# Performance work log

Hardware: AMD Instinct MI355X
Metric: run time of the kernel (lower is better)

## Reference

```python
import jax, jax.numpy as jnp
import numpy as np

KH = KW = 3          # kernel_size
PAD = 1              # padding (stride = 1)
K = KH * KW          # 9 kernel taps


def _bilinear_sample(x, ys, xs):
    """Bilinear sample with zero padding outside the image.
    x: [C,H,W]; ys, xs: [K,H,W] float sample coords. Returns [C,K,H,W]."""
    C, H, W = x.shape
    y0f = jnp.floor(ys)
    x0f = jnp.floor(xs)
    wy1 = ys - y0f
    wx1 = xs - x0f
    wy0 = 1.0 - wy1
    wx0 = 1.0 - wx1
    y0 = y0f.astype(jnp.int32)
    x0 = x0f.astype(jnp.int32)
    y1 = y0 + 1
    x1 = x0 + 1
    xf = x.reshape(C, H * W)

    def gather(yi, xi, wgt):
        valid = (yi >= 0) & (yi < H) & (xi >= 0) & (xi < W)
        idx = jnp.clip(yi, 0, H - 1) * W + jnp.clip(xi, 0, W - 1)  # [K,H,W]
        v = xf[:, idx.reshape(-1)].reshape(C, K, H, W)
        return v * (wgt * valid)[None]

    return (gather(y0, x0, wy0 * wx0) + gather(y0, x1, wy0 * wx1)
            + gather(y1, x0, wy1 * wx0) + gather(y1, x1, wy1 * wx1))


def _deform_conv2d(x, off, w):
    """DCNv1 for one (batch, group) slice.
    x: [C,H,W]; off: [2K,H,W] mmcv layout (dy,dx per tap); w: [Cout,Cin,KH,KW]."""
    C, H, W = x.shape
    off = off.reshape(K, 2, H, W)
    dy, dx = off[:, 0], off[:, 1]                       # [K,H,W]
    ky = (jnp.arange(K) // KW).astype(x.dtype)
    kx = (jnp.arange(K) % KW).astype(x.dtype)
    hh = jnp.arange(H, dtype=x.dtype)
    ww = jnp.arange(W, dtype=x.dtype)
    ys = dy + ky[:, None, None] - PAD + hh[None, :, None]   # stride=1
    xs = dx + kx[:, None, None] - PAD + ww[None, None, :]
    sampled = _bilinear_sample(x, ys, xs)               # [C,K,H,W]
    return jnp.einsum('ikhw,oik->ohw', sampled, w.reshape(w.shape[0], w.shape[1], K))


def reference(feat, offset, weight):
    """feat: [B,C,T,H,W]; offset: [B,2K,T,H,W]; weight: [T,Cout,Cin,KH,KW].
    groups=T, deform_groups=T -> each temporal slice is an independent DCN."""
    ft = jnp.transpose(feat, (0, 2, 1, 3, 4))    # [B,T,C,H,W]
    ot = jnp.transpose(offset, (0, 2, 1, 3, 4))  # [B,T,2K,H,W]
    per_t = jax.vmap(_deform_conv2d, in_axes=(0, 0, 0))       # over T (weight per-T)
    per_b = jax.vmap(per_t, in_axes=(0, 0, None))             # over B (weight shared)
    out = per_b(ft, ot, weight)                  # [B,T,C,H,W]
    return jnp.transpose(out, (0, 2, 1, 3, 4))   # [B,C,T,H,W]


def setup_inputs() -> dict:
    key = jax.random.key(0)
    k1, k2, k3 = jax.random.split(key, 3)
    B, C, T, H, W = 2, 32, 8, 192, 192
    feat = jax.random.normal(k1, (B, C, T, H, W), dtype=jnp.float32)
    offset = jax.random.normal(k2, (B, 2 * K, T, H, W), dtype=jnp.float32)
    weight = jax.random.normal(k3, (T, C, C, KH, KW), dtype=jnp.float32) * 0.05
    return {"feat": feat, "offset": offset, "weight": weight}
```

## Files before the change

### kernel.cpp

```cpp
#include <hip/hip_runtime.h>
#include <hip/hip_bf16.h>


#define CIN   32
#define COUT  32
#define TT    8
#define HH    192
#define WW    192
#define KK    9
#define HWSZ  (HH * WW)
#define PLANE (TT * HWSZ)

#define TILE_W 32
#define TILE_H 8
#define HALO   4
#define HROWS  (TILE_H + 2 * HALO + 1)
#define HCOLS  (TILE_W + 2 * HALO + 1)

typedef __attribute__((ext_vector_type(8))) short short8;
typedef __attribute__((ext_vector_type(4))) float f32x4;

union U4S8 { uint4 u; short8 s; };

__device__ __forceinline__ float bl_lo(uint u) { return __uint_as_float(u << 16); }
__device__ __forceinline__ float bl_hi(uint u) { return __uint_as_float(u & 0xffff0000u); }

__device__ __forceinline__ uint pk_bf16(float lo, float hi) {
    float2 p; p.x = lo; p.y = hi;
    __hip_bfloat162 b = __float22bfloat162_rn(p);
    union { __hip_bfloat162 b; uint u; } cv; cv.b = b;
    return cv.u;
}

__device__ __forceinline__ uint blerp_pack(uint a, uint b, uint c, uint d,
                                           float w00, float w01, float w10, float w11) {
    float lo = w00 * bl_lo(a) + w01 * bl_lo(b) + w10 * bl_lo(c) + w11 * bl_lo(d);
    float hi = w00 * bl_hi(a) + w01 * bl_hi(b) + w10 * bl_hi(c) + w11 * bl_hi(d);
    return pk_bf16(lo, hi);
}

__global__ __launch_bounds__(256) void transpose_bf16_kernel(
    const float* __restrict__ feat, uint* __restrict__ tf)
{
    __shared__ float tile[CIN][65];
    const int p0 = blockIdx.x * 64;
    const int t  = blockIdx.y;
    const int b  = blockIdx.z;

    const float* src = feat + (size_t)b * CIN * PLANE + (size_t)t * HWSZ + p0;
    #pragma unroll
    for (int it = 0; it < 8; ++it) {
        int i = it * 256 + threadIdx.x;
        int c = i >> 6, p = i & 63;
        tile[c][p] = src[(size_t)c * PLANE + p];
    }
    __syncthreads();

    uint* dst = tf + ((size_t)(b * TT + t) * HWSZ + p0) * (CIN / 2);
    #pragma unroll
    for (int it = 0; it < 4; ++it) {
        int i  = it * 256 + threadIdx.x;
        int p  = i >> 4, c2 = i & 15;
        dst[p * 16 + c2] = pk_bf16(tile[2 * c2][p], tile[2 * c2 + 1][p]);
    }
}

__global__ __launch_bounds__(256) void wprep_kernel(
    const float* __restrict__ wt, ushort* __restrict__ wfrag)
{
    int idx = blockIdx.x * 256 + threadIdx.x;
    if (idx >= TT * KK * 2 * 64 * 8) return;
    int t  = idx / (KK * 1024);
    int f  = idx % (KK * 1024);
    int k  = f >> 10;
    int r2 = f & 1023;
    int n    = r2 >> 9;
    int lane = (r2 >> 3) & 63;
    int j    = r2 & 7;
    int o = n * 16 + (lane & 15);
    int c = (lane >> 4) * 8 + j;
    float v = wt[(((size_t)t * COUT + o) * CIN + c) * KK + k];
    __hip_bfloat16 hb = __float2bfloat16(v);
    union { __hip_bfloat16 b; ushort u; } cv; cv.b = hb;
    wfrag[idx] = cv.u;
}

__global__ __launch_bounds__(256, 2) void dcn_mfma_kernel(
    const uint* __restrict__ tf,
    const float* __restrict__ offset,
    const ushort* __restrict__ wfrag,
    float* __restrict__ out)
{
    __shared__ uint4 halo[HROWS * HCOLS * 5];

    const int tid  = threadIdx.x;
    const int lane = tid & 63;
    const int wv   = tid >> 6;
    const int lane15 = lane & 15;
    const int quad   = lane >> 4;

    const int w0 = blockIdx.x * TILE_W;
    const int h0 = blockIdx.y * TILE_H;
    const int bt = blockIdx.z;
    const int t  = bt & (TT - 1);
    const int b  = bt >> 3;

    const int hlo = h0 - HALO, wlo = w0 - HALO;
    const int hhi = hlo + (HROWS - 1), whi = wlo + (HCOLS - 1);

    const uint4* tfs4 = (const uint4*)tf + (size_t)bt * HWSZ * 4;

    #pragma unroll
    for (int it = 0; it < 11; ++it) {
        int idx = it * 256 + tid;
        if (idx < HROWS * HCOLS * 4) {
            int r    = idx / (HCOLS * 4);
            int rem  = idx - r * (HCOLS * 4);
            int pv   = rem >> 2;
            int part = rem & 3;
            int gy = min(max(hlo + r, 0), HH - 1);
            int gx = min(max(wlo + pv, 0), WW - 1);
            halo[(r * HCOLS + pv) * 5 + part] = tfs4[(gy * WW + gx) * 4 + part];
        }
    }

    float offv[2 * KK];
    {
        const int orow = h0 + 2 * wv + (lane >> 5);
        const int ocol = w0 + (lane & 31);
        const float* offp = offset + (size_t)b * 2 * KK * PLANE
                          + (size_t)t * HWSZ + orow * WW + ocol;
        #pragma unroll
        for (int j = 0; j < 2 * KK; ++j) offv[j] = offp[(size_t)j * PLANE];
    }

    short8 bfr[KK][2];
    {
        const uint4* wfp = (const uint4*)(wfrag + (size_t)t * KK * 2 * 64 * 8);
        #pragma unroll
        for (int k = 0; k < KK; ++k)
            #pragma unroll
            for (int n = 0; n < 2; ++n) {
                U4S8 cv; cv.u = wfp[(k * 2 + n) * 64 + lane];
                bfr[k][n] = cv.s;
            }
    }

    __syncthreads();

    f32x4 acc[4][2];
    #pragma unroll
    for (int i = 0; i < 4; ++i)
        #pragma unroll
        for (int n = 0; n < 2; ++n) {
            acc[i][n][0] = 0.f; acc[i][n][1] = 0.f;
            acc[i][n][2] = 0.f; acc[i][n][3] = 0.f;
        }

    int own[4];
    #pragma unroll
    for (int i = 0; i < 4; ++i) own[i] = ((i >> 1) << 5) | ((i & 1) << 4) | lane15;

    #pragma unroll
    for (int k = 0; k < KK; ++k) {
        const int ky = k / 3 - 1;
        const int kx = k % 3 - 1;
        #pragma unroll
        for (int i = 0; i < 4; ++i) {
            const float dy = __shfl(offv[2 * k],     own[i], 64);
            const float dx = __shfl(offv[2 * k + 1], own[i], 64);
            const int hp = h0 + 2 * wv + (i >> 1);
            const int wp = w0 + ((i & 1) << 4) + lane15;

            const float ys = (float)(hp + ky) + dy;
            const float xs = (float)(wp + kx) + dx;
            const float y0f = floorf(ys), x0f = floorf(xs);
            const float wy1 = ys - y0f,  wx1 = xs - x0f;
            const float wy0 = 1.f - wy1, wx0 = 1.f - wx1;

            const int y0 = (int)y0f, x0i = (int)x0f;
            const int y1 = y0 + 1,   x1 = x0i + 1;

            const float vy0 = (y0 >= 0 && y0 < HH) ? 1.f : 0.f;
            const float vy1 = (y1 >= 0 && y1 < HH) ? 1.f : 0.f;
            const float vx0 = (x0i >= 0 && x0i < WW) ? 1.f : 0.f;
            const float vx1 = (x1 >= 0 && x1 < WW) ? 1.f : 0.f;

            const int cy0 = min(max(y0, 0), HH - 1);
            const int cy1 = min(max(y1, 0), HH - 1);
            const int cx0 = min(max(x0i, 0), WW - 1);
            const int cx1 = min(max(x1, 0), WW - 1);

            const float w00 = wy0 * wx0 * vy0 * vx0;
            const float w01 = wy0 * wx1 * vy0 * vx1;
            const float w10 = wy1 * wx0 * vy1 * vx0;
            const float w11 = wy1 * wx1 * vy1 * vx1;

            const bool inH = (cy0 >= hlo) & (cy1 <= hhi) & (cx0 >= wlo) & (cx1 <= whi);

            uint4 q00, q01, q10, q11;
            if (inH) {
                const int r0 = cy0 - hlo, r1 = cy1 - hlo;
                const int c0 = cx0 - wlo, c1 = cx1 - wlo;
                q00 = halo[(r0 * HCOLS + c0) * 5 + quad];
                q01 = halo[(r0 * HCOLS + c1) * 5 + quad];
                q10 = halo[(r1 * HCOLS + c0) * 5 + quad];
                q11 = halo[(r1 * HCOLS + c1) * 5 + quad];
            } else {
                q00 = tfs4[(cy0 * WW + cx0) * 4 + quad];
                q01 = tfs4[(cy0 * WW + cx1) * 4 + quad];
                q10 = tfs4[(cy1 * WW + cx0) * 4 + quad];
                q11 = tfs4[(cy1 * WW + cx1) * 4 + quad];
            }

            U4S8 af;
            af.u.x = blerp_pack(q00.x, q01.x, q10.x, q11.x, w00, w01, w10, w11);
            af.u.y = blerp_pack(q00.y, q01.y, q10.y, q11.y, w00, w01, w10, w11);
            af.u.z = blerp_pack(q00.z, q01.z, q10.z, q11.z, w00, w01, w10, w11);
            af.u.w = blerp_pack(q00.w, q01.w, q10.w, q11.w, w00, w01, w10, w11);

            acc[i][0] = __builtin_amdgcn_mfma_f32_16x16x32_bf16(af.s, bfr[k][0], acc[i][0], 0, 0, 0);
            acc[i][1] = __builtin_amdgcn_mfma_f32_16x16x32_bf16(af.s, bfr[k][1], acc[i][1], 0, 0, 0);
        }
    }

    float* ob = out + (size_t)b * COUT * PLANE + (size_t)t * HWSZ;
    #pragma unroll
    for (int i = 0; i < 4; ++i) {
        const int hp    = h0 + 2 * wv + (i >> 1);
        const int wbase = w0 + ((i & 1) << 4) + quad * 4;
        #pragma unroll
        for (int n = 0; n < 2; ++n) {
            const int o = n * 16 + lane15;
            float* op = ob + (size_t)o * PLANE + hp * WW + wbase;
            #pragma unroll
            for (int r = 0; r < 4; ++r) op[r] = acc[i][n][r];
        }
    }
}

__global__ __launch_bounds__(256) void dcn_fp32_kernel(
    const float* __restrict__ feat,
    const float* __restrict__ offset,
    const float* __restrict__ weight,
    float* __restrict__ out)
{
    __shared__ float sw[KK * CIN * COUT];
    const int tid = threadIdx.x;
    const int t   = blockIdx.y;
    const int b   = blockIdx.z;
    {
        const float* wg = weight + (size_t)t * (COUT * CIN * KK);
        #pragma unroll
        for (int j = 0; j < (KK * CIN * COUT) / 256; ++j) {
            int i  = tid + j * 256;
            int k  = i % KK;
            int oc = i / KK;
            sw[(k * CIN + (oc % CIN)) * COUT + (oc / CIN)] = wg[i];
        }
    }
    __syncthreads();

    const int pix = blockIdx.x * 256 + tid;
    const int h   = pix / WW;
    const int w   = pix % WW;

    float acc[COUT];
    #pragma unroll
    for (int o = 0; o < COUT; ++o) acc[o] = 0.0f;

    const float* offp = offset + ((size_t)(b * 2 * KK) * TT + t) * HWSZ + pix;
    float offv[2 * KK];
    #pragma unroll
    for (int j = 0; j < 2 * KK; ++j) offv[j] = offp[(size_t)j * PLANE];

    const float* fbase = feat + ((size_t)(b * CIN) * TT + t) * HWSZ;

    for (int k = 0; k < KK; ++k) {
        const float ys = (float)(h + k / 3 - 1) + offv[2 * k];
        const float xs = (float)(w + k % 3 - 1) + offv[2 * k + 1];
        const float y0f = floorf(ys), x0f = floorf(xs);
        const float wy1 = ys - y0f, wx1 = xs - x0f;
        const float wy0 = 1.0f - wy1, wx0 = 1.0f - wx1;
        const int y0 = (int)y0f, x0 = (int)x0f, y1 = y0 + 1, x1 = x0 + 1;
        const bool vy0 = (y0 >= 0) && (y0 < HH), vy1 = (y1 >= 0) && (y1 < HH);
        const bool vx0 = (x0 >= 0) && (x0 < WW), vx1 = (x1 >= 0) && (x1 < WW);
        const int cy0 = min(max(y0, 0), HH - 1), cy1 = min(max(y1, 0), HH - 1);
        const int cx0 = min(max(x0, 0), WW - 1), cx1 = min(max(x1, 0), WW - 1);
        const float w00 = wy0 * wx0 * ((vy0 && vx0) ? 1.0f : 0.0f);
        const float w01 = wy0 * wx1 * ((vy0 && vx1) ? 1.0f : 0.0f);
        const float w10 = wy1 * wx0 * ((vy1 && vx0) ? 1.0f : 0.0f);
        const float w11 = wy1 * wx1 * ((vy1 && vx1) ? 1.0f : 0.0f);
        const int i00 = cy0 * WW + cx0, i01 = cy0 * WW + cx1;
        const int i10 = cy1 * WW + cx0, i11 = cy1 * WW + cx1;

        const float*  sp   = fbase;
        const float4* wrow = (const float4*)&sw[k * CIN * COUT];
        for (int c = 0; c < CIN; ++c) {
            const float v = w00 * sp[i00] + w01 * sp[i01]
                          + w10 * sp[i10] + w11 * sp[i11];
            const float4* wp = wrow + c * (COUT / 4);
            #pragma unroll
            for (int o4 = 0; o4 < COUT / 4; ++o4) {
                const float4 wv = wp[o4];
                acc[4 * o4 + 0] += v * wv.x;
                acc[4 * o4 + 1] += v * wv.y;
                acc[4 * o4 + 2] += v * wv.z;
                acc[4 * o4 + 3] += v * wv.w;
            }
            sp += PLANE;
        }
    }

    float* op = out + ((size_t)(b * COUT) * TT + t) * HWSZ + pix;
    #pragma unroll
    for (int o = 0; o < COUT; ++o) op[(size_t)o * PLANE] = acc[o];
}

extern "C" void kernel_launch(void* const* d_in, const int* in_sizes, int n_in,
                              void* d_out, int out_size, void* d_ws, size_t ws_size,
                              hipStream_t stream) {
    const float* feat   = (const float*)d_in[0];
    const float* offset = (const float*)d_in[1];
    const float* weight = (const float*)d_in[2];
    float* out = (float*)d_out;

    const size_t tf_bytes = (size_t)2 * TT * HWSZ * CIN * sizeof(ushort);
    const size_t wf_bytes = (size_t)TT * KK * 2 * 64 * 8 * sizeof(ushort);

    if (ws_size >= tf_bytes + wf_bytes) {
        uint*   tf    = (uint*)d_ws;
        ushort* wfrag = (ushort*)((char*)d_ws + tf_bytes);

        transpose_bf16_kernel<<<dim3(HWSZ / 64, TT, 2), dim3(256), 0, stream>>>(feat, tf);
        wprep_kernel<<<dim3((TT * KK * 2 * 64 * 8 + 255) / 256), dim3(256), 0, stream>>>(weight, wfrag);
        dcn_mfma_kernel<<<dim3(WW / TILE_W, HH / TILE_H, 2 * TT), dim3(256), 0, stream>>>(
            tf, offset, wfrag, out);
    } else {
        dcn_fp32_kernel<<<dim3(HWSZ / 256, TT, 2), dim3(256), 0, stream>>>(feat, offset, weight, out);
    }
}
```

Baseline: 258.7 us.

## Compute bilinear coords once per pixel and share via LDS; raise occupancy

Each lane now computes the bilinear weights and packed halo addresses for exactly one pixel per tap. It writes them to shared memory, and the four lanes that need them for the MFMA A-fragment read them back, which removes the previous 4x redundant coordinate math and the offset shuffles. Offsets are prefetched one tap ahead and weight fragments are loaded per tap instead of held in registers. Both changes cut register pressure so launch bounds can target 3 blocks per CU. The halo is re-laid out as four channel planes, and the transpose kernel uses 256-pixel tiles. The costs are extra LDS traffic and per-tap global loads of weight fragments.

```diff
diff --git a/kernel.cpp b/kernel.cpp
--- a/kernel.cpp
+++ b/kernel.cpp
@@ -16,6 +16,9 @@
 #define HALO   4
 #define HROWS  (TILE_H + 2 * HALO + 1)
 #define HCOLS  (TILE_W + 2 * HALO + 1)
+#define HPLANE (HROWS * HCOLS)
+#define HPLANE_B (HPLANE * 16)
+#define HROW_B  (HCOLS * 16)
 
 typedef __attribute__((ext_vector_type(8))) short short8;
 typedef __attribute__((ext_vector_type(4))) float f32x4;
@@ -42,23 +45,20 @@
 __global__ __launch_bounds__(256) void transpose_bf16_kernel(
     const float* __restrict__ feat, uint* __restrict__ tf)
 {
-    __shared__ float tile[CIN][65];
-    const int p0 = blockIdx.x * 64;
+    __shared__ float tile[CIN][257];
+    const int p0 = blockIdx.x * 256;
     const int t  = blockIdx.y;
     const int b  = blockIdx.z;
 
     const float* src = feat + (size_t)b * CIN * PLANE + (size_t)t * HWSZ + p0;
     #pragma unroll
-    for (int it = 0; it < 8; ++it) {
-        int i = it * 256 + threadIdx.x;
-        int c = i >> 6, p = i & 63;
-        tile[c][p] = src[(size_t)c * PLANE + p];
-    }
+    for (int c = 0; c < CIN; ++c)
+        tile[c][threadIdx.x] = src[(size_t)c * PLANE + threadIdx.x];
     __syncthreads();
 
     uint* dst = tf + ((size_t)(b * TT + t) * HWSZ + p0) * (CIN / 2);
     #pragma unroll
-    for (int it = 0; it < 4; ++it) {
+    for (int it = 0; it < 16; ++it) {
         int i  = it * 256 + threadIdx.x;
         int p  = i >> 4, c2 = i & 15;
         dst[p * 16 + c2] = pk_bf16(tile[2 * c2][p], tile[2 * c2 + 1][p]);
@@ -85,13 +85,15 @@
     wfrag[idx] = cv.u;
 }
 
-__global__ __launch_bounds__(256, 2) void dcn_mfma_kernel(
+__global__ __launch_bounds__(256, 3) void dcn_mfma_kernel(
     const uint* __restrict__ tf,
     const float* __restrict__ offset,
     const ushort* __restrict__ wfrag,
     float* __restrict__ out)
 {
-    __shared__ uint4 halo[HROWS * HCOLS * 5];
+    __shared__ uint4 halo4[4 * HPLANE];
+    __shared__ f32x4 wts[256];
+    __shared__ uint2 meta2[256];
 
     const int tid  = threadIdx.x;
     const int lane = tid & 63;
@@ -113,40 +115,24 @@
     #pragma unroll
     for (int it = 0; it < 11; ++it) {
         int idx = it * 256 + tid;
-        if (idx < HROWS * HCOLS * 4) {
+        if (idx < 4 * HPLANE) {
             int r    = idx / (HCOLS * 4);
             int rem  = idx - r * (HCOLS * 4);
             int pv   = rem >> 2;
             int part = rem & 3;
             int gy = min(max(hlo + r, 0), HH - 1);
             int gx = min(max(wlo + pv, 0), WW - 1);
-            halo[(r * HCOLS + pv) * 5 + part] = tfs4[(gy * WW + gx) * 4 + part];
-        }
-    }
-
-    float offv[2 * KK];
-    {
-        const int orow = h0 + 2 * wv + (lane >> 5);
-        const int ocol = w0 + (lane & 31);
-        const float* offp = offset + (size_t)b * 2 * KK * PLANE
-                          + (size_t)t * HWSZ + orow * WW + ocol;
-        #pragma unroll
-        for (int j = 0; j < 2 * KK; ++j) offv[j] = offp[(size_t)j * PLANE];
-    }
-
-    short8 bfr[KK][2];
-    {
-        const uint4* wfp = (const uint4*)(wfrag + (size_t)t * KK * 2 * 64 * 8);
-        #pragma unroll
-        for (int k = 0; k < KK; ++k)
-            #pragma unroll
-            for (int n = 0; n < 2; ++n) {
-                U4S8 cv; cv.u = wfp[(k * 2 + n) * 64 + lane];
-                bfr[k][n] = cv.s;
-            }
-    }
-
-    __syncthreads();
+            halo4[part * HPLANE + r * HCOLS + pv] = tfs4[(gy * WW + gx) * 4 + part];
+        }
+    }
+
+    const int prow = h0 + 2 * wv + (lane >> 5);
+    const int pcol = w0 + (lane & 31);
+    const int px_own = (2 * wv + (lane >> 5)) * 32 + (lane & 31);
+    const float* offp = offset + (size_t)b * 2 * KK * PLANE + (size_t)t * HWSZ
+                      + prow * WW + pcol;
+
+    const uint4* wfp = (const uint4*)(wfrag + (size_t)t * KK * 2 * 64 * 8);
 
     f32x4 acc[4][2];
     #pragma unroll
@@ -157,23 +143,37 @@
             acc[i][n][2] = 0.f; acc[i][n][3] = 0.f;
         }
 
-    int own[4];
-    #pragma unroll
-    for (int i = 0; i < 4; ++i) own[i] = ((i >> 1) << 5) | ((i & 1) << 4) | lane15;
+    int pxc[4];
+    #pragma unroll
+    for (int i = 0; i < 4; ++i)
+        pxc[i] = (2 * wv + (i >> 1)) * 32 + ((i & 1) << 4) + lane15;
+
+    const uint qb = (uint)quad * HPLANE_B;
+    const char* hbase = (const char*)halo4;
+
+    __syncthreads();
+
+    float dy = offp[0];
+    float dx = offp[(size_t)PLANE];
 
     #pragma unroll
     for (int k = 0; k < KK; ++k) {
         const int ky = k / 3 - 1;
         const int kx = k % 3 - 1;
-        #pragma unroll
-        for (int i = 0; i < 4; ++i) {
-            const float dy = __shfl(offv[2 * k],     own[i], 64);
-            const float dx = __shfl(offv[2 * k + 1], own[i], 64);
-            const int hp = h0 + 2 * wv + (i >> 1);
-            const int wp = w0 + ((i & 1) << 4) + lane15;
-
-            const float ys = (float)(hp + ky) + dy;
-            const float xs = (float)(wp + kx) + dx;
+
+        float dyn = 0.f, dxn = 0.f;
+        if (k < KK - 1) {
+            dyn = offp[(size_t)(2 * k + 2) * PLANE];
+            dxn = offp[(size_t)(2 * k + 3) * PLANE];
+        }
+
+        U4S8 bf0, bf1;
+        bf0.u = wfp[(k * 2 + 0) * 64 + lane];
+        bf1.u = wfp[(k * 2 + 1) * 64 + lane];
+
+        {
+            const float ys = (float)(prow + ky) + dy;
+            const float xs = (float)(pcol + kx) + dx;
             const float y0f = floorf(ys), x0f = floorf(xs);
             const float wy1 = ys - y0f,  wx1 = xs - x0f;
             const float wy0 = 1.f - wy1, wx0 = 1.f - wx1;
@@ -191,22 +191,46 @@
             const int cx0 = min(max(x0i, 0), WW - 1);
             const int cx1 = min(max(x1, 0), WW - 1);
 
-            const float w00 = wy0 * wx0 * vy0 * vx0;
-            const float w01 = wy0 * wx1 * vy0 * vx1;
-            const float w10 = wy1 * wx0 * vy1 * vx0;
-            const float w11 = wy1 * wx1 * vy1 * vx1;
+            f32x4 w4;
+            w4[0] = wy0 * wx0 * vy0 * vx0;
+            w4[1] = wy0 * wx1 * vy0 * vx1;
+            w4[2] = wy1 * wx0 * vy1 * vx0;
+            w4[3] = wy1 * wx1 * vy1 * vx1;
 
             const bool inH = (cy0 >= hlo) & (cy1 <= hhi) & (cx0 >= wlo) & (cx1 <= whi);
+            uint mx;
+            if (inH) {
+                const int a00 = ((cy0 - hlo) * HCOLS + (cx0 - wlo)) * 16;
+                const int dcb = (cx1 - cx0) << 4;
+                const int drb = (cy1 - cy0) * HROW_B;
+                mx = (uint)a00 | ((uint)dcb << 14) | ((uint)drb << 19);
+            } else {
+                mx = 0x80000000u;
+            }
+            const uint my = (uint)cy0 | ((uint)cx0 << 8)
+                          | ((uint)cy1 << 16) | ((uint)cx1 << 24);
+
+            wts[px_own]   = w4;
+            meta2[px_own] = make_uint2(mx, my);
+        }
+
+        #pragma unroll
+        for (int i = 0; i < 4; ++i) {
+            const f32x4 w4  = wts[pxc[i]];
+            const uint2 mm  = meta2[pxc[i]];
 
             uint4 q00, q01, q10, q11;
-            if (inH) {
-                const int r0 = cy0 - hlo, r1 = cy1 - hlo;
-                const int c0 = cx0 - wlo, c1 = cx1 - wlo;
-                q00 = halo[(r0 * HCOLS + c0) * 5 + quad];
-                q01 = halo[(r0 * HCOLS + c1) * 5 + quad];
-                q10 = halo[(r1 * HCOLS + c0) * 5 + quad];
-                q11 = halo[(r1 * HCOLS + c1) * 5 + quad];
+            if ((int)mm.x >= 0) {
+                const uint a00 = (mm.x & 0x3fffu) + qb;
+                const uint dc  = (mm.x >> 14) & 0x1fu;
+                const uint dr  = (mm.x >> 19);
+                q00 = *(const uint4*)(hbase + a00);
+                q01 = *(const uint4*)(hbase + (a00 + dc));
+                q10 = *(const uint4*)(hbase + (a00 + dr));
+                q11 = *(const uint4*)(hbase + (a00 + dc + dr));
             } else {
+                const int cy0 = mm.y & 255,         cx0 = (mm.y >> 8) & 255;
+                const int cy1 = (mm.y >> 16) & 255, cx1 = mm.y >> 24;
                 q00 = tfs4[(cy0 * WW + cx0) * 4 + quad];
                 q01 = tfs4[(cy0 * WW + cx1) * 4 + quad];
                 q10 = tfs4[(cy1 * WW + cx0) * 4 + quad];
@@ -214,14 +238,16 @@
             }
 
             U4S8 af;
-            af.u.x = blerp_pack(q00.x, q01.x, q10.x, q11.x, w00, w01, w10, w11);
-            af.u.y = blerp_pack(q00.y, q01.y, q10.y, q11.y, w00, w01, w10, w11);
-            af.u.z = blerp_pack(q00.z, q01.z, q10.z, q11.z, w00, w01, w10, w11);
-            af.u.w = blerp_pack(q00.w, q01.w, q10.w, q11.w, w00, w01, w10, w11);
-
-            acc[i][0] = __builtin_amdgcn_mfma_f32_16x16x32_bf16(af.s, bfr[k][0], acc[i][0], 0, 0, 0);
-            acc[i][1] = __builtin_amdgcn_mfma_f32_16x16x32_bf16(af.s, bfr[k][1], acc[i][1], 0, 0, 0);
-        }
+            af.u.x = blerp_pack(q00.x, q01.x, q10.x, q11.x, w4[0], w4[1], w4[2], w4[3]);
+            af.u.y = blerp_pack(q00.y, q01.y, q10.y, q11.y, w4[0], w4[1], w4[2], w4[3]);
+            af.u.z = blerp_pack(q00.z, q01.z, q10.z, q11.z, w4[0], w4[1], w4[2], w4[3]);
+            af.u.w = blerp_pack(q00.w, q01.w, q10.w, q11.w, w4[0], w4[1], w4[2], w4[3]);
+
+            acc[i][0] = __builtin_amdgcn_mfma_f32_16x16x32_bf16(af.s, bf0.s, acc[i][0], 0, 0, 0);
+            acc[i][1] = __builtin_amdgcn_mfma_f32_16x16x32_bf16(af.s, bf1.s, acc[i][1], 0, 0, 0);
+        }
+
+        dy = dyn; dx = dxn;
     }
 
     float* ob = out + (size_t)b * COUT * PLANE + (size_t)t * HWSZ;
@@ -332,7 +358,7 @@
         uint*   tf    = (uint*)d_ws;
         ushort* wfrag = (ushort*)((char*)d_ws + tf_bytes);
 
-        transpose_bf16_kernel<<<dim3(HWSZ / 64, TT, 2), dim3(256), 0, stream>>>(feat, tf);
+        transpose_bf16_kernel<<<dim3(HWSZ / 256, TT, 2), dim3(256), 0, stream>>>(feat, tf);
         wprep_kernel<<<dim3((TT * KK * 2 * 64 * 8 + 255) / 256), dim3(256), 0, stream>>>(weight, wfrag);
         dcn_mfma_kernel<<<dim3(WW / TILE_W, HH / TILE_H, 2 * TT), dim3(256), 0, stream>>>(
             tf, offset, wfrag, out);
```

Result: faster. 248.2 us (-4.1%).
